# Optimization experiments

Measured on AMD Instinct MI355X. Metric: run time of the kernel, lower is better.

The kernel has to match this reference:

```python
import jax, jax.numpy as jnp
import numpy as np

IN_F = 4096
OUT_F = 4096
K = 16
THRESH = 0.0


def _group_ids():
    # consecutive chunks of size q = IN_F // K; last chunk absorbs remainder
    q, r = IN_F // K, IN_F % K
    ids = np.concatenate([np.full(q, k, np.int32) for k in range(K - 1)]
                         + [np.full(q + r, K - 1, np.int32)])
    return jnp.asarray(ids)


def setup_inputs() -> dict:
    key = jax.random.key(0)
    k1, k2, k3 = jax.random.split(key, 3)
    bound = 1.0 / np.sqrt(IN_F)
    x = jax.random.normal(k1, (8, 2048, IN_F), dtype=jnp.float32)
    weight = jax.random.uniform(k2, (OUT_F, IN_F), jnp.float32, -bound, bound)
    bias = jax.random.uniform(k3, (OUT_F,), jnp.float32, -bound, bound)
    return {"x": x, "weight": weight, "bias": bias}


def reference(x, weight, bias):
    B, T, F = x.shape
    xf = x.reshape(-1, F)                       # [N, F]
    # sum over output units of W @ x_chunk == colsum(W) . x_chunk
    wsum = jnp.sum(weight, axis=0)              # [F]
    contrib = xf * wsum[None, :]                # [N, F]
    gids = _group_ids()
    # group sums: [K, N] -> [N, K]
    g = jax.ops.segment_sum(contrib.T, gids, num_segments=K).T
    cs = jnp.cumsum(g, axis=1)                  # prefix activations [N, K]
    hit = cs >= THRESH
    idx = jnp.where(jnp.any(hit, axis=1), jnp.argmax(hit, axis=1), K - 1)
    S = jnp.take_along_axis(cs, idx[:, None], axis=1)  # [N, 1] scalar activation
    out = jax.nn.sigmoid(S + bias[None, :])     # [N, OUT_F]
    return out.reshape(B, T, OUT_F)
```

## Files before the change

kernel.cpp:

```cpp
#include <hip/hip_runtime.h>

#define IN_F 4096
#define OUT_F 4096
#define KGRP 16
#define N_ROWS (8 * 2048)

__global__ __launch_bounds__(256) void wsum_kernel(const float* __restrict__ w,
                                                   double* __restrict__ wsum) {
    const int f = blockIdx.x * 256 + threadIdx.x;
    const int r0 = blockIdx.y * 64;
    const float* p = w + (size_t)r0 * IN_F + f;
    double s = 0.0;
#pragma unroll 8
    for (int o = 0; o < 64; ++o) {
        s += (double)p[(size_t)o * IN_F];
    }
    atomicAdd(&wsum[f], s);
}

__global__ __launch_bounds__(256) void sigmaif_kernel(const float* __restrict__ x,
                                                      const float* __restrict__ bias,
                                                      const double* __restrict__ wsum,
                                                      float* __restrict__ out) {
    const int n = blockIdx.x;
    const int t = threadIdx.x;
    const int wave = t >> 6;

    const float4* xr = (const float4*)(x + (size_t)n * IN_F);

    __shared__ double g[KGRP];
    __shared__ float Sbc;

    double part[4];
#pragma unroll
    for (int k = 0; k < 4; ++k) {
        float4 v = xr[k * 256 + t];
        const double* wp = &wsum[4 * (k * 256 + t)];
        double2 w01 = *(const double2*)(wp);
        double2 w23 = *(const double2*)(wp + 2);
        part[k] = (double)v.x * w01.x + (double)v.y * w01.y +
                  (double)v.z * w23.x + (double)v.w * w23.y;
    }

#pragma unroll
    for (int k = 0; k < 4; ++k) {
#pragma unroll
        for (int off = 32; off > 0; off >>= 1)
            part[k] += __shfl_xor(part[k], off, 64);
        if ((t & 63) == 0) g[k * 4 + wave] = part[k];
    }
    __syncthreads();

    if (t == 0) {
        double cs = 0.0, S = 0.0;
        bool found = false;
#pragma unroll
        for (int k = 0; k < KGRP; ++k) {
            cs += g[k];
            if (!found && cs >= 0.0) { S = cs; found = true; }
        }
        if (!found) S = cs;
        Sbc = (float)S;
    }
    __syncthreads();

    const float S = Sbc;
    const float4* b4 = (const float4*)bias;
    float4* o4 = (float4*)(out + (size_t)n * OUT_F);
#pragma unroll
    for (int k = 0; k < 4; ++k) {
        float4 b = b4[k * 256 + t];
        float4 r;
        r.x = 1.0f / (1.0f + __expf(-(S + b.x)));
        r.y = 1.0f / (1.0f + __expf(-(S + b.y)));
        r.z = 1.0f / (1.0f + __expf(-(S + b.z)));
        r.w = 1.0f / (1.0f + __expf(-(S + b.w)));
        o4[k * 256 + t] = r;
    }
}

extern "C" void kernel_launch(void* const* d_in, const int* in_sizes, int n_in,
                              void* d_out, int out_size, void* d_ws, size_t ws_size,
                              hipStream_t stream) {
    const float* x    = (const float*)d_in[0];
    const float* w    = (const float*)d_in[1];
    const float* bias = (const float*)d_in[2];
    float* out = (float*)d_out;
    double* wsum = (double*)d_ws;

    hipMemsetAsync(d_ws, 0, IN_F * sizeof(double), stream);

    dim3 g1(IN_F / 256, OUT_F / 64);
    wsum_kernel<<<g1, 256, 0, stream>>>(w, wsum);

    sigmaif_kernel<<<N_ROWS, 256, 0, stream>>>(x, bias, wsum, out);
}
```

Measured before the change: 135.7 us.

## Split row kernel into reduce and output passes with nontemporal memory ops

Replaces the atomic column-sum with a two-stage partial-then-reduce scheme, which removes the memset and the atomics. Splits the fused per-row kernel into one kernel that computes the scalar activation per row and another that writes the sigmoid outputs. Uses nontemporal loads for x and nontemporal stores for the output to limit cache pollution from streaming data. The split adds two launches and a small intermediate buffer, and loses the overlap between reading x and writing the output inside one block.

```diff
diff --git a/kernel.cpp b/kernel.cpp
--- a/kernel.cpp
+++ b/kernel.cpp
@@ -5,36 +5,43 @@
 #define KGRP 16
 #define N_ROWS (8 * 2048)
 
-__global__ __launch_bounds__(256) void wsum_kernel(const float* __restrict__ w,
-                                                   double* __restrict__ wsum) {
+typedef float f32x4 __attribute__((ext_vector_type(4)));
+
+
+__global__ __launch_bounds__(256) void wsum_partial_kernel(const float* __restrict__ w,
+                                                           double* __restrict__ partial) {
     const int f = blockIdx.x * 256 + threadIdx.x;
-    const int r0 = blockIdx.y * 64;
+    const int r0 = blockIdx.y * 256;
     const float* p = w + (size_t)r0 * IN_F + f;
     double s = 0.0;
 #pragma unroll 8
-    for (int o = 0; o < 64; ++o) {
-        s += (double)p[(size_t)o * IN_F];
-    }
-    atomicAdd(&wsum[f], s);
+    for (int o = 0; o < 256; ++o) s += (double)p[(size_t)o * IN_F];
+    partial[blockIdx.y * IN_F + f] = s;
 }
 
-__global__ __launch_bounds__(256) void sigmaif_kernel(const float* __restrict__ x,
-                                                      const float* __restrict__ bias,
-                                                      const double* __restrict__ wsum,
-                                                      float* __restrict__ out) {
+__global__ __launch_bounds__(256) void wsum_reduce_kernel(const double* __restrict__ partial,
+                                                          double* __restrict__ wsum) {
+    const int f = blockIdx.x * 256 + threadIdx.x;
+    double s = 0.0;
+#pragma unroll
+    for (int p = 0; p < KGRP; ++p) s += partial[p * IN_F + f];
+    wsum[f] = s;
+}
+
+__global__ __launch_bounds__(256) void srow_kernel(const float* __restrict__ x,
+                                                   const double* __restrict__ wsum,
+                                                   float* __restrict__ S) {
     const int n = blockIdx.x;
     const int t = threadIdx.x;
     const int wave = t >> 6;
-
-    const float4* xr = (const float4*)(x + (size_t)n * IN_F);
+    const f32x4* xr = (const f32x4*)(x + (size_t)n * IN_F);
 
     __shared__ double g[KGRP];
-    __shared__ float Sbc;
 
     double part[4];
 #pragma unroll
     for (int k = 0; k < 4; ++k) {
-        float4 v = xr[k * 256 + t];
+        f32x4 v = __builtin_nontemporal_load(&xr[k * 256 + t]);
         const double* wp = &wsum[4 * (k * 256 + t)];
         double2 w01 = *(const double2*)(wp);
         double2 w23 = *(const double2*)(wp + 2);
@@ -52,30 +59,35 @@
     __syncthreads();
 
     if (t == 0) {
-        double cs = 0.0, S = 0.0;
+        double cs = 0.0, Sv = 0.0;
         bool found = false;
 #pragma unroll
         for (int k = 0; k < KGRP; ++k) {
             cs += g[k];
-            if (!found && cs >= 0.0) { S = cs; found = true; }
+            if (!found && cs >= 0.0) { Sv = cs; found = true; }
         }
-        if (!found) S = cs;
-        Sbc = (float)S;
+        if (!found) Sv = cs;
+        S[n] = (float)Sv;
     }
-    __syncthreads();
+}
 
-    const float S = Sbc;
-    const float4* b4 = (const float4*)bias;
-    float4* o4 = (float4*)(out + (size_t)n * OUT_F);
+__global__ __launch_bounds__(256) void out_kernel(const float* __restrict__ S,
+                                                  const float* __restrict__ bias,
+                                                  float* __restrict__ out) {
+    const int n = blockIdx.x;
+    const int t = threadIdx.x;
+    const float Sv = S[n];
+    const f32x4* b4 = (const f32x4*)bias;
+    f32x4* o4 = (f32x4*)(out + (size_t)n * OUT_F);
 #pragma unroll
     for (int k = 0; k < 4; ++k) {
-        float4 b = b4[k * 256 + t];
-        float4 r;
-        r.x = 1.0f / (1.0f + __expf(-(S + b.x)));
-        r.y = 1.0f / (1.0f + __expf(-(S + b.y)));
-        r.z = 1.0f / (1.0f + __expf(-(S + b.z)));
-        r.w = 1.0f / (1.0f + __expf(-(S + b.w)));
-        o4[k * 256 + t] = r;
+        f32x4 b = b4[k * 256 + t];
+        f32x4 r;
+        r.x = 1.0f / (1.0f + __expf(-(Sv + b.x)));
+        r.y = 1.0f / (1.0f + __expf(-(Sv + b.y)));
+        r.z = 1.0f / (1.0f + __expf(-(Sv + b.z)));
+        r.w = 1.0f / (1.0f + __expf(-(Sv + b.w)));
+        __builtin_nontemporal_store(r, &o4[k * 256 + t]);
     }
 }
 
@@ -86,12 +98,15 @@
     const float* w    = (const float*)d_in[1];
     const float* bias = (const float*)d_in[2];
     float* out = (float*)d_out;
-    double* wsum = (double*)d_ws;
 
-    hipMemsetAsync(d_ws, 0, IN_F * sizeof(double), stream);
+    char* ws = (char*)d_ws;
+    double* wsum    = (double*)(ws);
+    float*  S       = (float*)(ws + 32 * 1024);
+    double* partial = (double*)(ws + 96 * 1024);
 
-    dim3 g1(IN_F / 256, OUT_F / 64);
-    wsum_kernel<<<g1, 256, 0, stream>>>(w, wsum);
-
-    sigmaif_kernel<<<N_ROWS, 256, 0, stream>>>(x, bias, wsum, out);
+    dim3 g1(IN_F / 256, KGRP);
+    wsum_partial_kernel<<<g1, 256, 0, stream>>>(w, partial);
+    wsum_reduce_kernel<<<IN_F / 256, 256, 0, stream>>>(partial, wsum);
+    srow_kernel<<<N_ROWS, 256, 0, stream>>>(x, wsum, S);
+    out_kernel<<<N_ROWS, 256, 0, stream>>>(S, bias, out);
 }
```

Measured after the change: 122.3 us. 1.11x faster.
